# Optimization experiments

Measured on AMD Instinct MI355X. Metric: run time of the kernel, lower is better.

The kernel has to match this reference:

```python
import jax, jax.numpy as jnp
import numpy as np

M, K, N = 4096, 7168, 18432  # tokens, in_features, out_features


def setup_inputs() -> dict:
    key = jax.random.key(0)
    kx, kw, ks = jax.random.split(key, 3)
    x = jax.random.normal(kx, (M, K), dtype=jnp.float32)
    # int8 quantized weight, layout [in_features, out_features] as in the torch module
    weight = jax.random.randint(kw, (K, N), -128, 128, dtype=jnp.int8)
    # per-output-channel dequant scale (bf16 in the original; fp32 here for a stable baseline)
    scale = jax.random.uniform(ks, (N,), dtype=jnp.float32) * 0.02 + 1e-3
    return {"x": x, "weight": weight, "scale": scale}


def reference(x, weight, scale):
    # Fused dequant + GEMM: y = x @ (int8_weight * scale_per_out_channel)
    w = weight.astype(x.dtype) * scale.astype(x.dtype)[None, :]  # [K, N]
    return x @ w  # [M, N]
```

## Files before the change

### kernel.cpp

```cpp
#include <hip/hip_runtime.h>
#include <hip/hip_bf16.h>
#include <cstdint>
#include <cstddef>

#define M_ 4096
#define K_ 7168
#define N_ 18432
#define NT 112

typedef __attribute__((ext_vector_type(4))) int i32x4;
typedef __attribute__((ext_vector_type(16))) int i32x16;

#define AS1 __attribute__((address_space(1)))
#define AS3 __attribute__((address_space(3)))

__device__ __forceinline__ void gld_lds16(void* lds, const void* g) {
  __builtin_amdgcn_global_load_lds((const AS1 void*)g, (AS3 void*)lds, 16, 0, 0);
}

__global__ __launch_bounds__(256) void quant_x_kernel(const float* __restrict__ x,
                                                      signed char* __restrict__ xq,
                                                      float* __restrict__ sx) {
  const int m = blockIdx.x;
  const float4* row4 = (const float4*)(x + (size_t)m * K_);
  float mx = 0.f;
  for (int i = threadIdx.x; i < K_ / 4; i += 256) {
    float4 v = row4[i];
    mx = fmaxf(mx, fmaxf(fmaxf(fabsf(v.x), fabsf(v.y)), fmaxf(fabsf(v.z), fabsf(v.w))));
  }
#pragma unroll
  for (int d = 1; d < 64; d <<= 1) mx = fmaxf(mx, __shfl_xor(mx, d));
  __shared__ float wred[4];
  if ((threadIdx.x & 63) == 0) wred[threadIdx.x >> 6] = mx;
  __syncthreads();
  mx = fmaxf(fmaxf(wred[0], wred[1]), fmaxf(wred[2], wred[3]));
  const float inv = mx > 0.f ? 127.f / mx : 0.f;
  if (threadIdx.x == 0) sx[m] = mx / 127.f;
  char4* q4 = (char4*)(xq + (size_t)m * K_);
  for (int i = threadIdx.x; i < K_ / 4; i += 256) {
    float4 v = row4[i];
    char4 c;
    c.x = (signed char)__float2int_rn(v.x * inv);
    c.y = (signed char)__float2int_rn(v.y * inv);
    c.z = (signed char)__float2int_rn(v.z * inv);
    c.w = (signed char)__float2int_rn(v.w * inv);
    q4[i] = c;
  }
}

__global__ __launch_bounds__(256) void transpose_w_kernel(const int* __restrict__ W,
                                                          signed char* __restrict__ Wt) {
  __shared__ __align__(16) signed char t[64][80];
  const int k0 = blockIdx.x * 64;
  const int n0 = blockIdx.y * 64;
  const int r = threadIdx.x >> 4;
  const int c4 = (threadIdx.x & 15) * 4;
#pragma unroll
  for (int rr = 0; rr < 4; ++rr) {
    const int row = rr * 16 + r;
    int4 v = *(const int4*)(W + (size_t)(k0 + row) * N_ + n0 + c4);
    t[c4 + 0][row] = (signed char)v.x;
    t[c4 + 1][row] = (signed char)v.y;
    t[c4 + 2][row] = (signed char)v.z;
    t[c4 + 3][row] = (signed char)v.w;
  }
  __syncthreads();
  const int nr = threadIdx.x >> 2;
  const int cb = (threadIdx.x & 3) * 16;
  int4 o = *(const int4*)&t[nr][cb];
  *(int4*)(Wt + (size_t)(n0 + nr) * K_ + k0 + cb) = o;
}

__global__ __launch_bounds__(512, 2) void gemm_i8_kernel(const signed char* __restrict__ Aq,
                                                         const signed char* __restrict__ Bt,
                                                         const float* __restrict__ sx,
                                                         const float* __restrict__ scale,
                                                         float* __restrict__ C) {
  __shared__ __align__(16) signed char lds[65536];

  const int bid = blockIdx.x;
  const int xcd = bid & 7;
  const int j = bid >> 3;
  const int m0 = (j & 15) * 256;
  const int n0 = (xcd * 9 + (j >> 4)) * 256;

  const int tid = threadIdx.x;
  const int w = tid >> 6;
  const int lane = tid & 63;
  const int wr = w >> 2;
  const int wc = w & 3;

  const int fr32 = lane & 31;
  const int kh = lane >> 5;
  const int sw = (fr32 >> 2) & 3;
  const int ps0 = ((kh ^ sw) << 4);
  const int ps1 = ps0 ^ 0x20;
  const int rA = (wr * 128 + fr32) * 64;
  const int rB = 16384 + (wc * 64 + fr32) * 64;

  const int ls16 = (((lane & 3) ^ ((lane >> 4) & 3)) << 4);
  const int pr0 = w * 16 + (lane >> 2);
  const unsigned offA0 = (unsigned)(m0 + pr0) * K_ + ls16;
  const unsigned offA1 = (unsigned)(m0 + 128 + pr0) * K_ + ls16;
  const unsigned offB0 = (unsigned)(n0 + pr0) * K_ + ls16;
  const unsigned offB1 = (unsigned)(n0 + 128 + pr0) * K_ + ls16;

#define STAGE(T, P) do {                                                           \
    const int tc_ = (T) < NT ? (T) : NT - 1;                                       \
    signed char* dA_ = lds + (P) * 32768 + w * 1024;                               \
    gld_lds16(dA_, Aq + (size_t)offA0 + tc_ * 64);                                 \
    gld_lds16(dA_ + 8192, Aq + (size_t)offA1 + tc_ * 64);                          \
    signed char* dB_ = dA_ + 16384;                                                \
    gld_lds16(dB_, Bt + (size_t)offB0 + tc_ * 64);                                 \
    gld_lds16(dB_ + 8192, Bt + (size_t)offB1 + tc_ * 64);                          \
  } while (0)
#define LDFR(FA, FB, P, KST) do {                                                  \
    const signed char* base_ = lds + (P) * 32768 + ((KST) ? ps1 : ps0);            \
    _Pragma("unroll") for (int mt_ = 0; mt_ < 4; ++mt_)                            \
      FA[mt_] = *(const i32x4*)(base_ + rA + mt_ * 2048);                          \
    _Pragma("unroll") for (int nt_ = 0; nt_ < 2; ++nt_)                            \
      FB[nt_] = *(const i32x4*)(base_ + rB + nt_ * 2048);                          \
  } while (0)
#define MFMA8(FA, FB) do {                                                         \
    __builtin_amdgcn_s_setprio(1);                                                 \
    _Pragma("unroll") for (int mt_ = 0; mt_ < 4; ++mt_)                            \
    _Pragma("unroll") for (int nt_ = 0; nt_ < 2; ++nt_)                            \
      acc[mt_][nt_] = __builtin_amdgcn_mfma_i32_32x32x32_i8(                       \
          FA[mt_], FB[nt_], acc[mt_][nt_], 0, 0, 0);                               \
    __builtin_amdgcn_s_setprio(0);                                                 \
  } while (0)
#define BAR do { asm volatile("" ::: "memory");                                    \
                 __builtin_amdgcn_s_barrier();                                     \
                 asm volatile("" ::: "memory"); } while (0)
#define VM0 asm volatile("s_waitcnt vmcnt(0)" ::: "memory")
#define LGKM0 asm volatile("s_waitcnt lgkmcnt(0)" ::: "memory")
#define SB __builtin_amdgcn_sched_barrier(0)

#define KTILE(P, T) do {                                                           \
    STAGE((T) + 2, P); SB;                                                         \
    MFMA8(fA0, fB0); LDFR(fA0, fB0, (P) ^ 1, 0); SB;                               \
    MFMA8(fA1, fB1); LDFR(fA1, fB1, (P) ^ 1, 1); SB;                               \
    VM0;                        \
    BAR;                      \
  } while (0)

  i32x16 acc[4][2] = {};
  i32x4 fA0[4], fB0[2], fA1[4], fB1[2];

  STAGE(0, 0); STAGE(1, 1);
  VM0;
  BAR;
  LDFR(fA0, fB0, 0, 0); LDFR(fA1, fB1, 0, 1);
  LGKM0; SB;
  BAR;

  for (int t = 0; t < NT; t += 2) {
    KTILE(0, t);
    KTILE(1, t + 1);
  }

  const int mb = m0 + wr * 128;
  const int nb = n0 + wc * 64;
  const int col = lane & 31;
  const int rhi = (lane >> 5) * 4;
  const float scl0 = scale[nb + col];
  const float scl1 = scale[nb + 32 + col];
#pragma unroll
  for (int mt = 0; mt < 4; ++mt) {
#pragma unroll
    for (int r = 0; r < 16; ++r) {
      const int row = mb + mt * 32 + (r & 3) + (r >> 2) * 8 + rhi;
      const float s = sx[row];
      float* out = C + (size_t)row * N_ + nb + col;
      out[0]  = (float)acc[mt][0][r] * s * scl0;
      out[32] = (float)acc[mt][1][r] * s * scl1;
    }
  }
#undef STAGE
#undef LDFR
#undef MFMA8
#undef BAR
#undef VM0
#undef LGKM0
#undef SB
#undef KTILE
}

__global__ __launch_bounds__(256) void fb_gemm_kernel(const float* __restrict__ X,
                                                      const int* __restrict__ W,
                                                      const float* __restrict__ scale,
                                                      float* __restrict__ Y) {
  __shared__ float xs[16][65];
  __shared__ float ws_[16][65];
  const int bn = blockIdx.x * 64;
  const int bm = blockIdx.y * 64;
  const int tx = threadIdx.x & 15;
  const int ty = threadIdx.x >> 4;
  float acc[4][4] = {};
  for (int k0 = 0; k0 < K_; k0 += 16) {
    for (int i = threadIdx.x; i < 64 * 16; i += 256) {
      int r = i >> 4, c = i & 15;
      xs[c][r] = X[(size_t)(bm + r) * K_ + k0 + c];
    }
    for (int i = threadIdx.x; i < 16 * 64; i += 256) {
      int r = i >> 6, c = i & 63;
      ws_[r][c] = (float)W[(size_t)(k0 + r) * N_ + bn + c];
    }
    __syncthreads();
#pragma unroll
    for (int kk = 0; kk < 16; ++kk) {
      float a[4], b[4];
#pragma unroll
      for (int i = 0; i < 4; ++i) a[i] = xs[kk][ty * 4 + i];
#pragma unroll
      for (int j = 0; j < 4; ++j) b[j] = ws_[kk][tx * 4 + j];
#pragma unroll
      for (int i = 0; i < 4; ++i)
#pragma unroll
        for (int j = 0; j < 4; ++j) acc[i][j] += a[i] * b[j];
    }
    __syncthreads();
  }
#pragma unroll
  for (int i = 0; i < 4; ++i)
#pragma unroll
    for (int j = 0; j < 4; ++j)
      Y[(size_t)(bm + ty * 4 + i) * N_ + bn + tx * 4 + j] = acc[i][j] * scale[bn + tx * 4 + j];
}

extern "C" void kernel_launch(void* const* d_in, const int* in_sizes, int n_in,
                              void* d_out, int out_size, void* d_ws, size_t ws_size,
                              hipStream_t stream) {
  const float* x = (const float*)d_in[0];
  const int* w = (const int*)d_in[1];
  const float* scale = (const float*)d_in[2];
  float* y = (float*)d_out;

  const size_t xq_bytes = (size_t)M_ * K_;
  const size_t sx_off = xq_bytes;
  const size_t wt_off = sx_off + (size_t)M_ * 4;
  const size_t need = wt_off + (size_t)N_ * K_;

  if (ws_size >= need) {
    signed char* xq = (signed char*)d_ws;
    float* sx = (float*)((char*)d_ws + sx_off);
    signed char* wt = (signed char*)((char*)d_ws + wt_off);
    hipLaunchKernelGGL(quant_x_kernel, dim3(M_), dim3(256), 0, stream, x, xq, sx);
    hipLaunchKernelGGL(transpose_w_kernel, dim3(K_ / 64, N_ / 64), dim3(256), 0, stream, w, wt);
    hipLaunchKernelGGL(gemm_i8_kernel, dim3((M_ / 256) * (N_ / 256)), dim3(512), 0, stream,
                       xq, wt, sx, scale, y);
  } else {
    hipLaunchKernelGGL(fb_gemm_kernel, dim3(N_ / 64, M_ / 64), dim3(256), 0, stream,
                       x, w, scale, y);
  }
}
```

Measured before the change: 787.3 us.

## Deepen int8 GEMM LDS pipeline to four stages with scheduled MFMA/DS interleave

Grows the GEMM kernel's LDS ring from two to four 32 KB stages and prefetches three K-tiles ahead. This lets each iteration wait with vmcnt(4) instead of draining all global-to-LDS loads. The main loop is unrolled by four with rotating buffer indices. sched_group_barrier sequences interleave MFMAs with LDS fragment reads and global loads, and the s_setprio wrapping is removed. The aim is to hide global latency better, at the cost of 128 KB LDS per block, which likely allows only one block per CU instead of the two the launch bounds request.

After: 735.1 us. 1.07x faster.

```diff
diff --git a/kernel.cpp b/kernel.cpp
--- a/kernel.cpp
+++ b/kernel.cpp
@@ -76,7 +76,7 @@
                                                          const float* __restrict__ sx,
                                                          const float* __restrict__ scale,
                                                          float* __restrict__ C) {
-  __shared__ __align__(16) signed char lds[65536];
+  __shared__ __align__(16) signed char lds[131072];
 
   const int bid = blockIdx.x;
   const int xcd = bid & 7;
@@ -122,41 +122,48 @@
       FB[nt_] = *(const i32x4*)(base_ + rB + nt_ * 2048);                          \
   } while (0)
 #define MFMA8(FA, FB) do {                                                         \
-    __builtin_amdgcn_s_setprio(1);                                                 \
     _Pragma("unroll") for (int mt_ = 0; mt_ < 4; ++mt_)                            \
     _Pragma("unroll") for (int nt_ = 0; nt_ < 2; ++nt_)                            \
       acc[mt_][nt_] = __builtin_amdgcn_mfma_i32_32x32x32_i8(                       \
           FA[mt_], FB[nt_], acc[mt_][nt_], 0, 0, 0);                               \
-    __builtin_amdgcn_s_setprio(0);                                                 \
   } while (0)
 #define BAR do { asm volatile("" ::: "memory");                                    \
                  __builtin_amdgcn_s_barrier();                                     \
                  asm volatile("" ::: "memory"); } while (0)
-#define VM0 asm volatile("s_waitcnt vmcnt(0)" ::: "memory")
-#define LGKM0 asm volatile("s_waitcnt lgkmcnt(0)" ::: "memory")
-#define SB __builtin_amdgcn_sched_barrier(0)
-
-#define KTILE(P, T) do {                                                           \
-    STAGE((T) + 2, P); SB;                                                         \
-    MFMA8(fA0, fB0); LDFR(fA0, fB0, (P) ^ 1, 0); SB;                               \
-    MFMA8(fA1, fB1); LDFR(fA1, fB1, (P) ^ 1, 1); SB;                               \
-    VM0;                        \
-    BAR;                      \
+#define VM4 asm volatile("s_waitcnt vmcnt(4)" ::: "memory")
+#define SGB(M, N) __builtin_amdgcn_sched_group_barrier((M), (N), 0)
+#define SGBPROG do {                                                               \
+    SGB(0x10, 4);                                             \
+    SGB(0x8, 2); SGB(0x100, 1); SGB(0x8, 2); SGB(0x100, 1);                        \
+    SGB(0x8, 2); SGB(0x100, 1); SGB(0x8, 2); SGB(0x100, 1);         \
+    SGB(0x100, 2);                                                       \
+    SGB(0x8, 2); SGB(0x100, 1); SGB(0x8, 2); SGB(0x100, 1);                        \
+    SGB(0x8, 2); SGB(0x100, 1); SGB(0x8, 2); SGB(0x100, 1);         \
+    SGB(0x100, 2);                                                       \
+  } while (0)
+
+#define KTILE(T, BUFN, BUFS) do {                                                  \
+    STAGE((T) + 3, BUFS);                                                          \
+    MFMA8(fA0, fB0); LDFR(fA0, fB0, BUFN, 0);                                      \
+    MFMA8(fA1, fB1); LDFR(fA1, fB1, BUFN, 1);                                      \
+    SGBPROG;                                                                       \
+    VM4;                       \
+    BAR;                                                                           \
   } while (0)
 
   i32x16 acc[4][2] = {};
   i32x4 fA0[4], fB0[2], fA1[4], fB1[2];
 
-  STAGE(0, 0); STAGE(1, 1);
-  VM0;
+  STAGE(0, 0); STAGE(1, 1); STAGE(2, 2);
+  VM4;
   BAR;
   LDFR(fA0, fB0, 0, 0); LDFR(fA1, fB1, 0, 1);
-  LGKM0; SB;
-  BAR;
-
-  for (int t = 0; t < NT; t += 2) {
-    KTILE(0, t);
-    KTILE(1, t + 1);
+
+  for (int t = 0; t < NT; t += 4) {
+    KTILE(t, 1, 3);
+    KTILE(t + 1, 2, 0);
+    KTILE(t + 2, 3, 1);
+    KTILE(t + 3, 0, 2);
   }
 
   const int mb = m0 + wr * 128;
@@ -180,9 +187,9 @@
 #undef LDFR
 #undef MFMA8
 #undef BAR
-#undef VM0
-#undef LGKM0
-#undef SB
+#undef VM4
+#undef SGB
+#undef SGBPROG
 #undef KTILE
 }
 
```
